# Optimization experiments

Measured on AMD Instinct MI355X. Metric: run time of the kernel, lower is better.

Reference implementation:

```python
import jax, jax.numpy as jnp
import numpy as np

B, SQ, SK, D, H = 4, 2048, 2048, 1024, 16
EPS = 1e-6  # flax LayerNorm default


def layer_norm(x, g, b):
    m = x.mean(-1, keepdims=True)
    var = ((x - m) ** 2).mean(-1, keepdims=True)
    return (x - m) * jax.lax.rsqrt(var + EPS) * g + b


def setup_inputs() -> dict:
    key = jax.random.key(0)
    ks = jax.random.split(key, 16)
    s = 1.0 / np.sqrt(D).astype(np.float32)
    inp = {
        'q': jax.random.normal(ks[0], (B, SQ, D), jnp.float32),
        'k': jax.random.normal(ks[1], (B, SK, D), jnp.float32),
        'v': jax.random.normal(ks[2], (B, SK, D), jnp.float32),
        'mask': jax.random.randint(ks[3], (B, SK), 0, 2).astype(bool),
        'Wq': jax.random.normal(ks[4], (D, D), jnp.float32) * s,
        'bq': jnp.zeros((D,), jnp.float32),
        'Wk': jax.random.normal(ks[5], (D, D), jnp.float32) * s,
        'bk': jnp.zeros((D,), jnp.float32),
        'Wv': jax.random.normal(ks[6], (D, D), jnp.float32) * s,
        'bv': jnp.zeros((D,), jnp.float32),
        'Wo': jax.random.normal(ks[7], (D, D), jnp.float32) * s,
        'bo': jnp.zeros((D,), jnp.float32),
        'g1': jnp.ones((D,), jnp.float32),
        'b1': jnp.zeros((D,), jnp.float32),
        'g2': jnp.ones((D,), jnp.float32),
        'b2': jnp.zeros((D,), jnp.float32),
    }
    return inp


def reference(q, k, v, mask, Wq, bq, Wk, bk, Wv, bv, Wo, bo, g1, b1, g2, b2):
    qp = q @ Wq + bq                      # [B, SQ, D]
    kp = k @ Wk + bk                      # [B, SK, D]
    vp = v @ Wv + bv
    qh = qp.reshape(B, SQ, H, D // H)     # head = slice of last dim (matches scatter)
    kh = kp.reshape(B, SK, H, D // H)
    vh = vp.reshape(B, SK, H, D // H)
    # NOTE: original scales by sqrt(dim_out) (full dim), not head dim
    logits = jnp.einsum('bqhd,bkhd->bhqk', qh, kh) / np.sqrt(D).astype(np.float32)
    m = mask[:, None, None, :]            # [B,1,1,SK] broadcast over heads & queries
    A = jax.nn.softmax(jnp.where(m, logits, -jnp.inf), axis=-1)
    A = jnp.where(jnp.isnan(A), 0.0, A)   # fully-masked rows -> 0 (as in original)
    attn = jnp.einsum('bhqk,bkhd->bqhd', A, vh).reshape(B, SQ, D)  # gather heads
    x = layer_norm(qp + attn, g1, b1)
    out = layer_norm(x + jax.nn.relu(x @ Wo + bo), g2, b2)
    return out
```

## Files before the change

kernel.cpp:

```cpp
#include <hip/hip_runtime.h>

#define B_   4
#define SQS  2048
#define SKS  2048
#define DM   1024
#define H_   16
#define MT   8192

typedef __attribute__((ext_vector_type(8))) short bf16x8;
typedef __attribute__((ext_vector_type(4))) float f32x4;

__device__ __forceinline__ float bf2f(unsigned int u) { return __uint_as_float(u << 16); }
__device__ __forceinline__ unsigned short f2bf(float f) {
  unsigned int u = __float_as_uint(f);
  return (unsigned short)((u + 0x7fffu + ((u >> 16) & 1u)) >> 16);
}
__device__ __forceinline__ unsigned int pk_bf16(float a, float b) {
  return __builtin_amdgcn_perm(__float_as_uint(b) + 0x8000u,
                               __float_as_uint(a) + 0x8000u, 0x07060302u);
}
__device__ __forceinline__ void async16(const void* g, void* l) {
  __builtin_amdgcn_global_load_lds((const __attribute__((address_space(1))) unsigned int*)g,
                                   (__attribute__((address_space(3))) unsigned int*)l,
                                   16, 0, 0);
}

__global__ __launch_bounds__(256)
void cvt3_kernel(const float* __restrict__ a, const float* __restrict__ b,
                 const float* __restrict__ c,
                 unsigned short* __restrict__ oa, unsigned short* __restrict__ ob,
                 unsigned short* __restrict__ oc)
{
  const float* src = (blockIdx.y == 0) ? a : (blockIdx.y == 1) ? b : c;
  unsigned short* dst = (blockIdx.y == 0) ? oa : (blockIdx.y == 1) ? ob : oc;
  size_t i = ((size_t)blockIdx.x * 256 + threadIdx.x) * 4;
  float4 f = *(const float4*)(src + i);
  uint2 o;
  o.x = (unsigned)f2bf(f.x) | ((unsigned)f2bf(f.y) << 16);
  o.y = (unsigned)f2bf(f.z) | ((unsigned)f2bf(f.w) << 16);
  *(uint2*)(dst + i) = o;
}

__global__ __launch_bounds__(256)
void wtrans_kernel(const float* __restrict__ w0, const float* __restrict__ w1,
                   const float* __restrict__ w2, const float* __restrict__ w3,
                   unsigned short* __restrict__ t0, unsigned short* __restrict__ t1,
                   unsigned short* __restrict__ t2, unsigned short* __restrict__ t3)
{
  const float* W = (blockIdx.z == 0) ? w0 : (blockIdx.z == 1) ? w1 : (blockIdx.z == 2) ? w2 : w3;
  unsigned short* Wt = (blockIdx.z == 0) ? t0 : (blockIdx.z == 1) ? t1 : (blockIdx.z == 2) ? t2 : t3;
  __shared__ float s[32][33];
  int n0 = blockIdx.x * 32, k0 = blockIdx.y * 32;
  int tid = threadIdx.x;
#pragma unroll
  for (int p = 0; p < 4; p++) {
    int idx = p * 256 + tid;
    int r = idx >> 5, c = idx & 31;
    s[r][c] = W[(size_t)(k0 + r) * DM + n0 + c];
  }
  __syncthreads();
#pragma unroll
  for (int p = 0; p < 4; p++) {
    int idx = p * 256 + tid;
    int r = idx >> 5, c = idx & 31;
    Wt[(size_t)(n0 + r) * DM + k0 + c] = f2bf(s[c][r]);
  }
}

__global__ __launch_bounds__(256)
void mkbias_kernel(const int* __restrict__ m, float* __restrict__ bias)
{
  int i = blockIdx.x * 256 + threadIdx.x;
  bias[i] = m[i] ? 0.0f : -1e30f;
}

__global__ __launch_bounds__(256)
void qkv_gemm(const unsigned short* __restrict__ A0, const unsigned short* __restrict__ A1,
              const unsigned short* __restrict__ A2,
              const unsigned short* __restrict__ W0, const unsigned short* __restrict__ W1,
              const unsigned short* __restrict__ W2,
              const float* __restrict__ s0, const float* __restrict__ s1,
              const float* __restrict__ s2,
              unsigned short* __restrict__ o0, unsigned short* __restrict__ o1,
              unsigned short* __restrict__ o2)
{
  const int z = blockIdx.z;
  const unsigned short* A  = (z == 0) ? A0 : (z == 1) ? A1 : A2;
  const unsigned short* Wt = (z == 0) ? W0 : (z == 1) ? W1 : W2;
  const float* bias        = (z == 0) ? s0 : (z == 1) ? s1 : s2;
  unsigned short* C        = (z == 0) ? o0 : (z == 1) ? o1 : o2;

  __shared__ short As[128 * 32];
  __shared__ short Bs[128 * 32];
  const int tid = threadIdx.x;
  const int m0 = blockIdx.y * 128, n0 = blockIdx.x * 128;
  const int wave = tid >> 6, ln = tid & 15, qd = (tid & 63) >> 4;
  const int wm = (wave >> 1) * 64, wn = (wave & 1) * 64;
  const int cA = tid, cB = 256 + tid;
  const int arA = cA >> 2, acA = (cA & 3) * 8;
  const int arB = cB >> 2, acB = (cB & 3) * 8;

  f32x4 acc[4][4];
  const f32x4 vzero = {0.f, 0.f, 0.f, 0.f};
#pragma unroll
  for (int i = 0; i < 4; i++)
#pragma unroll
    for (int j = 0; j < 4; j++) acc[i][j] = vzero;

  for (int k0 = 0; k0 < DM; k0 += 32) {
    __syncthreads();
    async16(A  + (size_t)(m0 + arA) * DM + k0 + acA, (char*)As + cA * 16);
    async16(A  + (size_t)(m0 + arB) * DM + k0 + acB, (char*)As + cB * 16);
    async16(Wt + (size_t)(n0 + arA) * DM + k0 + acA, (char*)Bs + cA * 16);
    async16(Wt + (size_t)(n0 + arB) * DM + k0 + acB, (char*)Bs + cB * 16);
    __syncthreads();

    bf16x8 af[4], bfr[4];
#pragma unroll
    for (int i = 0; i < 4; i++)
      af[i] = *(const bf16x8*)(As + (wm + i * 16 + ln) * 32 + qd * 8);
#pragma unroll
    for (int j = 0; j < 4; j++)
      bfr[j] = *(const bf16x8*)(Bs + (wn + j * 16 + ln) * 32 + qd * 8);
#pragma unroll
    for (int i = 0; i < 4; i++)
#pragma unroll
      for (int j = 0; j < 4; j++)
        acc[i][j] = __builtin_amdgcn_mfma_f32_16x16x32_bf16(af[i], bfr[j], acc[i][j], 0, 0, 0);
  }

#pragma unroll
  for (int j = 0; j < 4; j++) {
    int col = n0 + wn + j * 16 + ln;
    float bj = bias[col];
#pragma unroll
    for (int i = 0; i < 4; i++) {
      int row = m0 + wm + i * 16 + qd * 4;
#pragma unroll
      for (int r = 0; r < 4; r++)
        C[(size_t)(row + r) * DM + col] = f2bf(acc[i][j][r] + bj);
    }
  }
}

__global__ __launch_bounds__(256)
void gemm_bf16(const unsigned short* __restrict__ A,
               const unsigned short* __restrict__ Wt,
               const float* __restrict__ bias,
               unsigned short* __restrict__ C,
               int relu)
{
  __shared__ short As[128 * 32];
  __shared__ short Bs[128 * 32];
  const int tid = threadIdx.x;
  const int m0 = blockIdx.y * 128, n0 = blockIdx.x * 128;
  const int wave = tid >> 6, ln = tid & 15, qd = (tid & 63) >> 4;
  const int wm = (wave >> 1) * 64, wn = (wave & 1) * 64;
  const int cA = tid, cB = 256 + tid;
  const int arA = cA >> 2, acA = (cA & 3) * 8;
  const int arB = cB >> 2, acB = (cB & 3) * 8;

  f32x4 acc[4][4];
  const f32x4 vzero = {0.f, 0.f, 0.f, 0.f};
#pragma unroll
  for (int i = 0; i < 4; i++)
#pragma unroll
    for (int j = 0; j < 4; j++) acc[i][j] = vzero;

  for (int k0 = 0; k0 < DM; k0 += 32) {
    __syncthreads();
    async16(A  + (size_t)(m0 + arA) * DM + k0 + acA, (char*)As + cA * 16);
    async16(A  + (size_t)(m0 + arB) * DM + k0 + acB, (char*)As + cB * 16);
    async16(Wt + (size_t)(n0 + arA) * DM + k0 + acA, (char*)Bs + cA * 16);
    async16(Wt + (size_t)(n0 + arB) * DM + k0 + acB, (char*)Bs + cB * 16);
    __syncthreads();

    bf16x8 af[4], bfr[4];
#pragma unroll
    for (int i = 0; i < 4; i++)
      af[i] = *(const bf16x8*)(As + (wm + i * 16 + ln) * 32 + qd * 8);
#pragma unroll
    for (int j = 0; j < 4; j++)
      bfr[j] = *(const bf16x8*)(Bs + (wn + j * 16 + ln) * 32 + qd * 8);
#pragma unroll
    for (int i = 0; i < 4; i++)
#pragma unroll
      for (int j = 0; j < 4; j++)
        acc[i][j] = __builtin_amdgcn_mfma_f32_16x16x32_bf16(af[i], bfr[j], acc[i][j], 0, 0, 0);
  }

#pragma unroll
  for (int j = 0; j < 4; j++) {
    int col = n0 + wn + j * 16 + ln;
    float bj = bias[col];
#pragma unroll
    for (int i = 0; i < 4; i++) {
      int row = m0 + wm + i * 16 + qd * 4;
#pragma unroll
      for (int r = 0; r < 4; r++) {
        float v = acc[i][j][r] + bj;
        if (relu) v = fmaxf(v, 0.f);
        C[(size_t)(row + r) * DM + col] = f2bf(v);
      }
    }
  }
}

__global__ __launch_bounds__(256)
void vtrans_kernel(const unsigned short* __restrict__ vp, unsigned short* __restrict__ vT)
{
  __shared__ unsigned short s[64][68];
  int b = blockIdx.z, h = blockIdx.y, k0 = blockIdx.x * 64;
  int tid = threadIdx.x;
#pragma unroll
  for (int p = 0; p < 4; p++) {
    int c = p * 256 + tid;
    int k = c >> 4, d0 = (c & 15) * 4;
    uint2 u = *(const uint2*)(vp + (size_t)(b * SKS + k0 + k) * DM + (h << 6) + d0);
    *(uint2*)(&s[k][d0]) = u;
  }
  __syncthreads();
#pragma unroll
  for (int p = 0; p < 4; p++) {
    int c = p * 256 + tid;
    int d = c >> 4, m = c & 15;
    int t  = ((m & 1) << 1) | (m >> 3);
    int qd = (m >> 1) & 3;
    int ks = t * 16 + qd * 4;
    unsigned short r0 = s[ks + 0][d];
    unsigned short r1 = s[ks + 1][d];
    unsigned short r2 = s[ks + 2][d];
    unsigned short r3 = s[ks + 3][d];
    uint2 u;
    u.x = (unsigned)r0 | ((unsigned)r1 << 16);
    u.y = (unsigned)r2 | ((unsigned)r3 << 16);
    *(uint2*)(vT + (size_t)((b * H_ + h) * 64 + d) * SKS + k0 + m * 4) = u;
  }
}

__global__ __launch_bounds__(256, 4)
void attn_fwd(const unsigned short* __restrict__ qp,
              const unsigned short* __restrict__ kp,
              const unsigned short* __restrict__ vT,
              const float* __restrict__ maskb,
              unsigned short* __restrict__ attn)
{
  __shared__ short Ks[64 * 64];
  __shared__ short Vs[64 * 64];
  __shared__ float bias_s[64];

  const int tid = threadIdx.x;
  const int b = blockIdx.z, h = blockIdx.y, q0 = blockIdx.x * 128;
  const int wave = tid >> 6, ln = tid & 15, qd = (tid & 63) >> 4;
  const int cA = tid, cB = 256 + tid;
  const int rA = cA >> 3, jgA = ((cA & 7) ^ (rA & 7)) * 8;
  const int rB = cB >> 3, jgB = ((cB & 7) ^ (rB & 7)) * 8;
  const float SCALE = 0.03125f;

  const unsigned short* kbase = kp + (size_t)(b * SKS) * DM + (h << 6);
  const unsigned short* vbase = vT + (size_t)((b * H_ + h) * 64) * SKS;

  const unsigned short* qrow = qp + (size_t)(b * SQS + q0 + wave * 32 + ln) * DM + (h << 6);
  bf16x8 qf[2][2];
  qf[0][0] = *(const bf16x8*)(qrow + qd * 8);
  qf[0][1] = *(const bf16x8*)(qrow + 32 + qd * 8);
  qf[1][0] = *(const bf16x8*)(qrow + 16 * DM + qd * 8);
  qf[1][1] = *(const bf16x8*)(qrow + 16 * DM + 32 + qd * 8);

  const f32x4 vzero = {0.f, 0.f, 0.f, 0.f};
  f32x4 oA[2][4];
#pragma unroll
  for (int g = 0; g < 2; g++)
#pragma unroll
    for (int t = 0; t < 4; t++) oA[g][t] = vzero;
  float lr[2] = {0.f, 0.f};

  for (int kt = 0; kt < SKS / 64; kt++) {
    const int k0 = kt * 64;
    __syncthreads();
    if (tid < 64) bias_s[tid] = maskb[b * SKS + k0 + tid];
    async16(kbase + (size_t)(k0 + rA) * DM + jgA, (char*)Ks + cA * 16);
    async16(kbase + (size_t)(k0 + rB) * DM + jgB, (char*)Ks + cB * 16);
    async16(vbase + (size_t)rA * SKS + k0 + jgA, (char*)Vs + cA * 16);
    async16(vbase + (size_t)rB * SKS + k0 + jgB, (char*)Vs + cB * 16);
    __syncthreads();

    f32x4 sS[2][4];
#pragma unroll
    for (int t = 0; t < 4; t++) {
      const short* krow = Ks + (t * 16 + ln) * 64;
      bf16x8 kf0 = *(const bf16x8*)(krow + ((0 + qd) ^ (ln & 7)) * 8);
      bf16x8 kf1 = *(const bf16x8*)(krow + ((4 + qd) ^ (ln & 7)) * 8);
      f32x4 a0 = __builtin_amdgcn_mfma_f32_16x16x32_bf16(kf0, qf[0][0], vzero, 0, 0, 0);
      a0       = __builtin_amdgcn_mfma_f32_16x16x32_bf16(kf1, qf[0][1], a0,    0, 0, 0);
      f32x4 a1 = __builtin_amdgcn_mfma_f32_16x16x32_bf16(kf0, qf[1][0], vzero, 0, 0, 0);
      a1       = __builtin_amdgcn_mfma_f32_16x16x32_bf16(kf1, qf[1][1], a1,    0, 0, 0);
      sS[0][t] = a0;
      sS[1][t] = a1;
    }

    bf16x8 pf[2][2];
#pragma unroll
    for (int g = 0; g < 2; g++) {
      float p[4][4];
      float acc = 0.f;
#pragma unroll
      for (int t = 0; t < 4; t++) {
        float4 bt = *(const float4*)(bias_s + t * 16 + qd * 4);
        p[t][0] = __expf(fmaf(sS[g][t][0], SCALE, bt.x));
        p[t][1] = __expf(fmaf(sS[g][t][1], SCALE, bt.y));
        p[t][2] = __expf(fmaf(sS[g][t][2], SCALE, bt.z));
        p[t][3] = __expf(fmaf(sS[g][t][3], SCALE, bt.w));
        acc += (p[t][0] + p[t][1]) + (p[t][2] + p[t][3]);
      }
      lr[g] += acc;
      union { bf16x8 v; unsigned int u[4]; } P0, P1;
      P0.u[0] = pk_bf16(p[0][0], p[0][1]);
      P0.u[1] = pk_bf16(p[0][2], p[0][3]);
      P0.u[2] = pk_bf16(p[2][0], p[2][1]);
      P0.u[3] = pk_bf16(p[2][2], p[2][3]);
      P1.u[0] = pk_bf16(p[1][0], p[1][1]);
      P1.u[1] = pk_bf16(p[1][2], p[1][3]);
      P1.u[2] = pk_bf16(p[3][0], p[3][1]);
      P1.u[3] = pk_bf16(p[3][2], p[3][3]);
      pf[g][0] = P0.v;
      pf[g][1] = P1.v;
    }

#pragma unroll
    for (int t2 = 0; t2 < 4; t2++) {
      const short* vrow = Vs + (t2 * 16 + ln) * 64;
#pragma unroll
      for (int kk = 0; kk < 2; kk++) {
        bf16x8 vf = *(const bf16x8*)(vrow + ((kk * 4 + qd) ^ (ln & 7)) * 8);
        oA[0][t2] = __builtin_amdgcn_mfma_f32_16x16x32_bf16(pf[0][kk], vf, oA[0][t2], 0, 0, 0);
        oA[1][t2] = __builtin_amdgcn_mfma_f32_16x16x32_bf16(pf[1][kk], vf, oA[1][t2], 0, 0, 0);
      }
    }
  }

#pragma unroll
  for (int g = 0; g < 2; g++) {
    float l = lr[g];
    l += __shfl_xor(l, 16);
    l += __shfl_xor(l, 32);
    float linv[4];
#pragma unroll
    for (int r = 0; r < 4; r++) {
      float lq = __shfl(l, qd * 4 + r);
      linv[r] = (lq > 0.f) ? 1.0f / lq : 0.f;
    }
#pragma unroll
    for (int t2 = 0; t2 < 4; t2++)
#pragma unroll
      for (int r = 0; r < 4; r++) {
        size_t idx = (size_t)(b * SQS + q0 + wave * 32 + g * 16 + qd * 4 + r) * DM
                   + (h << 6) + t2 * 16 + ln;
        attn[idx] = f2bf(oA[g][t2][r] * linv[r]);
      }
  }
}

__global__ __launch_bounds__(256)
void ln_fuse(const unsigned short* __restrict__ Xa, const unsigned short* __restrict__ Xb,
             const float* __restrict__ gamma, const float* __restrict__ beta,
             unsigned short* __restrict__ outb, float* __restrict__ outf, int mode)
{
  const int row = blockIdx.x, tid = threadIdx.x;
  const size_t base = (size_t)row * DM + tid * 4;
  uint2 ua = *(const uint2*)(Xa + base);
  uint2 ub = *(const uint2*)(Xb + base);
  float v0 = bf2f(ua.x & 0xffffu) + bf2f(ub.x & 0xffffu);
  float v1 = bf2f(ua.x >> 16)     + bf2f(ub.x >> 16);
  float v2 = bf2f(ua.y & 0xffffu) + bf2f(ub.y & 0xffffu);
  float v3 = bf2f(ua.y >> 16)     + bf2f(ub.y >> 16);
  float s  = (v0 + v1) + (v2 + v3);
  float s2 = (v0 * v0 + v1 * v1) + (v2 * v2 + v3 * v3);
#pragma unroll
  for (int off = 1; off < 64; off <<= 1) {
    s  += __shfl_xor(s, off);
    s2 += __shfl_xor(s2, off);
  }
  __shared__ float red[8];
  if ((tid & 63) == 0) { red[tid >> 6] = s; red[4 + (tid >> 6)] = s2; }
  __syncthreads();
  float S  = (red[0] + red[1]) + (red[2] + red[3]);
  float S2 = (red[4] + red[5]) + (red[6] + red[7]);
  float mean = S * (1.0f / 1024.0f);
  float var  = S2 * (1.0f / 1024.0f) - mean * mean;
  float rstd = rsqrtf(var + 1e-6f);
  int c = tid * 4;
  float o0 = (v0 - mean) * rstd * gamma[c + 0] + beta[c + 0];
  float o1 = (v1 - mean) * rstd * gamma[c + 1] + beta[c + 1];
  float o2 = (v2 - mean) * rstd * gamma[c + 2] + beta[c + 2];
  float o3 = (v3 - mean) * rstd * gamma[c + 3] + beta[c + 3];
  if (mode == 0) {
    uint2 o;
    o.x = (unsigned)f2bf(o0) | ((unsigned)f2bf(o1) << 16);
    o.y = (unsigned)f2bf(o2) | ((unsigned)f2bf(o3) << 16);
    *(uint2*)(outb + base) = o;
  } else {
    float4 o = {o0, o1, o2, o3};
    *(float4*)(outf + base) = o;
  }
}

extern "C" void kernel_launch(void* const* d_in, const int* in_sizes, int n_in,
                              void* d_out, int out_size, void* d_ws, size_t ws_size,
                              hipStream_t stream)
{
  (void)in_sizes; (void)n_in; (void)out_size; (void)ws_size;
  const float* q    = (const float*)d_in[0];
  const float* k    = (const float*)d_in[1];
  const float* v    = (const float*)d_in[2];
  const int*   mask = (const int*)  d_in[3];
  const float* Wq   = (const float*)d_in[4];
  const float* bq   = (const float*)d_in[5];
  const float* Wk   = (const float*)d_in[6];
  const float* bk   = (const float*)d_in[7];
  const float* Wv   = (const float*)d_in[8];
  const float* bv   = (const float*)d_in[9];
  const float* Wo   = (const float*)d_in[10];
  const float* bo   = (const float*)d_in[11];
  const float* g1   = (const float*)d_in[12];
  const float* b1   = (const float*)d_in[13];
  const float* g2   = (const float*)d_in[14];
  const float* b2   = (const float*)d_in[15];

  char* ws = (char*)d_ws;
  const size_t SZ16 = (size_t)16 << 20;
  unsigned short* qi   = (unsigned short*)(ws + 0 * SZ16);
  unsigned short* ki   = (unsigned short*)(ws + 1 * SZ16);
  unsigned short* vi   = (unsigned short*)(ws + 2 * SZ16);
  unsigned short* qpb  = (unsigned short*)(ws + 3 * SZ16);
  unsigned short* kpb  = (unsigned short*)(ws + 4 * SZ16);
  unsigned short* vpb  = (unsigned short*)(ws + 5 * SZ16);
  unsigned short* vTb  = (unsigned short*)(ws + 6 * SZ16);
  unsigned short* Wqt  = (unsigned short*)(ws + 7 * SZ16 + ((size_t)0 << 20));
  unsigned short* Wkt  = (unsigned short*)(ws + 7 * SZ16 + ((size_t)2 << 20));
  unsigned short* Wvt  = (unsigned short*)(ws + 7 * SZ16 + ((size_t)4 << 20));
  unsigned short* Wot  = (unsigned short*)(ws + 7 * SZ16 + ((size_t)6 << 20));
  float*          mskb = (float*)         (ws + 7 * SZ16 + ((size_t)8 << 20));
  unsigned short* attnb = qi;
  unsigned short* xb    = ki;
  unsigned short* hb    = vi;

  cvt3_kernel  <<<dim3(8192, 3),    256, 0, stream>>>(q, k, v, qi, ki, vi);
  wtrans_kernel<<<dim3(32, 32, 4),  256, 0, stream>>>(Wq, Wk, Wv, Wo, Wqt, Wkt, Wvt, Wot);
  mkbias_kernel<<<32,               256, 0, stream>>>(mask, mskb);

  qkv_gemm     <<<dim3(8, 64, 3),   256, 0, stream>>>(qi, ki, vi, Wqt, Wkt, Wvt,
                                                      bq, bk, bv, qpb, kpb, vpb);

  vtrans_kernel<<<dim3(32, 16, 4),  256, 0, stream>>>(vpb, vTb);
  attn_fwd     <<<dim3(16, 16, 4),  256, 0, stream>>>(qpb, kpb, vTb, mskb, attnb);

  ln_fuse      <<<8192,             256, 0, stream>>>(qpb, attnb, g1, b1, xb, nullptr, 0);
  gemm_bf16    <<<dim3(8, 64),      256, 0, stream>>>(xb, Wot, bo, hb, 1);
  ln_fuse      <<<8192,             256, 0, stream>>>(xb, hb, g2, b2, nullptr, (float*)d_out, 1);
}
```

Before: 391.1 us.

## Widen GEMM and attention K-tiles, fold scale into K projection, use exp2

Doubles the K-step of both GEMMs to 64 with an XOR-swizzled LDS layout, and doubles the attention key tile to 128 per iteration. This halves the number of barrier round trips. The softmax scale and log2(e) are folded into the K projection output and the mask bias. The bias is injected as the MFMA accumulator init, so the kernel can use native exp2 and truncating bf16 packing. Row sums are now computed with an MFMA against a ones vector instead of shuffle reductions. Truncating P to bf16 and computing the row sum from bf16 values change numerics slightly. The bigger tiles raise LDS use per block.

New measurement: 374.4 us. 1.04x faster.

```diff
diff --git a/kernel.cpp b/kernel.cpp
--- a/kernel.cpp
+++ b/kernel.cpp
@@ -15,15 +15,24 @@
   unsigned int u = __float_as_uint(f);
   return (unsigned short)((u + 0x7fffu + ((u >> 16) & 1u)) >> 16);
 }
-__device__ __forceinline__ unsigned int pk_bf16(float a, float b) {
-  return __builtin_amdgcn_perm(__float_as_uint(b) + 0x8000u,
-                               __float_as_uint(a) + 0x8000u, 0x07060302u);
+__device__ __forceinline__ unsigned int pk_trunc(float a, float b) {
+  return __builtin_amdgcn_perm(__float_as_uint(b), __float_as_uint(a), 0x07060302u);
+}
+__device__ __forceinline__ float fexp2(float x) {
+#if __has_builtin(__builtin_amdgcn_exp2f)
+  return __builtin_amdgcn_exp2f(x);
+#else
+  return __expf(x * 0.69314718056f);
+#endif
 }
 __device__ __forceinline__ void async16(const void* g, void* l) {
   __builtin_amdgcn_global_load_lds((const __attribute__((address_space(1))) unsigned int*)g,
                                    (__attribute__((address_space(3))) unsigned int*)l,
                                    16, 0, 0);
 }
+
+#define KSCALE 0.0450842200f
+#define BIAS_UNMASKED 0.0028151213f
 
 __global__ __launch_bounds__(256)
 void cvt3_kernel(const float* __restrict__ a, const float* __restrict__ b,
@@ -71,7 +80,7 @@
 void mkbias_kernel(const int* __restrict__ m, float* __restrict__ bias)
 {
   int i = blockIdx.x * 256 + threadIdx.x;
-  bias[i] = m[i] ? 0.0f : -1e30f;
+  bias[i] = m[i] ? BIAS_UNMASKED : -1e30f;
 }
 
 __global__ __launch_bounds__(256)
@@ -89,16 +98,22 @@
   const unsigned short* Wt = (z == 0) ? W0 : (z == 1) ? W1 : W2;
   const float* bias        = (z == 0) ? s0 : (z == 1) ? s1 : s2;
   unsigned short* C        = (z == 0) ? o0 : (z == 1) ? o1 : o2;
-
-  __shared__ short As[128 * 32];
-  __shared__ short Bs[128 * 32];
+  const float sc           = (z == 1) ? KSCALE : 1.0f;
+
+  __shared__ short As[128 * 64];
+  __shared__ short Bs[128 * 64];
   const int tid = threadIdx.x;
   const int m0 = blockIdx.y * 128, n0 = blockIdx.x * 128;
   const int wave = tid >> 6, ln = tid & 15, qd = (tid & 63) >> 4;
   const int wm = (wave >> 1) * 64, wn = (wave & 1) * 64;
-  const int cA = tid, cB = 256 + tid;
-  const int arA = cA >> 2, acA = (cA & 3) * 8;
-  const int arB = cB >> 2, acB = (cB & 3) * 8;
+
+  int srow[4], sgj[4];
+#pragma unroll
+  for (int u = 0; u < 4; u++) {
+    int c = u * 256 + tid;
+    srow[u] = c >> 3;
+    sgj[u] = ((c & 7) ^ (srow[u] & 7)) * 8;
+  }
 
   f32x4 acc[4][4];
   const f32x4 vzero = {0.f, 0.f, 0.f, 0.f};
@@ -107,26 +122,32 @@
 #pragma unroll
     for (int j = 0; j < 4; j++) acc[i][j] = vzero;
 
-  for (int k0 = 0; k0 < DM; k0 += 32) {
+  for (int k0 = 0; k0 < DM; k0 += 64) {
     __syncthreads();
-    async16(A  + (size_t)(m0 + arA) * DM + k0 + acA, (char*)As + cA * 16);
-    async16(A  + (size_t)(m0 + arB) * DM + k0 + acB, (char*)As + cB * 16);
-    async16(Wt + (size_t)(n0 + arA) * DM + k0 + acA, (char*)Bs + cA * 16);
-    async16(Wt + (size_t)(n0 + arB) * DM + k0 + acB, (char*)Bs + cB * 16);
+#pragma unroll
+    for (int u = 0; u < 4; u++) {
+      int c = u * 256 + tid;
+      async16(A  + (size_t)(m0 + srow[u]) * DM + k0 + sgj[u], (char*)As + c * 16);
+      async16(Wt + (size_t)(n0 + srow[u]) * DM + k0 + sgj[u], (char*)Bs + c * 16);
+    }
     __syncthreads();
 
-    bf16x8 af[4], bfr[4];
-#pragma unroll
-    for (int i = 0; i < 4; i++)
-      af[i] = *(const bf16x8*)(As + (wm + i * 16 + ln) * 32 + qd * 8);
-#pragma unroll
-    for (int j = 0; j < 4; j++)
-      bfr[j] = *(const bf16x8*)(Bs + (wn + j * 16 + ln) * 32 + qd * 8);
-#pragma unroll
-    for (int i = 0; i < 4; i++)
+#pragma unroll
+    for (int kk = 0; kk < 2; kk++) {
+      const int ch = ((kk * 4 + qd) ^ (ln & 7)) * 8;
+      bf16x8 af[4], bfr[4];
+#pragma unroll
+      for (int i = 0; i < 4; i++)
+        af[i] = *(const bf16x8*)(As + (wm + i * 16 + ln) * 64 + ch);
 #pragma unroll
       for (int j = 0; j < 4; j++)
-        acc[i][j] = __builtin_amdgcn_mfma_f32_16x16x32_bf16(af[i], bfr[j], acc[i][j], 0, 0, 0);
+        bfr[j] = *(const bf16x8*)(Bs + (wn + j * 16 + ln) * 64 + ch);
+#pragma unroll
+      for (int i = 0; i < 4; i++)
+#pragma unroll
+        for (int j = 0; j < 4; j++)
+          acc[i][j] = __builtin_amdgcn_mfma_f32_16x16x32_bf16(af[i], bfr[j], acc[i][j], 0, 0, 0);
+    }
   }
 
 #pragma unroll
@@ -138,7 +159,7 @@
       int row = m0 + wm + i * 16 + qd * 4;
 #pragma unroll
       for (int r = 0; r < 4; r++)
-        C[(size_t)(row + r) * DM + col] = f2bf(acc[i][j][r] + bj);
+        C[(size_t)(row + r) * DM + col] = f2bf((acc[i][j][r] + bj) * sc);
     }
   }
 }
@@ -150,15 +171,20 @@
                unsigned short* __restrict__ C,
                int relu)
 {
-  __shared__ short As[128 * 32];
-  __shared__ short Bs[128 * 32];
+  __shared__ short As[128 * 64];
+  __shared__ short Bs[128 * 64];
   const int tid = threadIdx.x;
   const int m0 = blockIdx.y * 128, n0 = blockIdx.x * 128;
   const int wave = tid >> 6, ln = tid & 15, qd = (tid & 63) >> 4;
   const int wm = (wave >> 1) * 64, wn = (wave & 1) * 64;
-  const int cA = tid, cB = 256 + tid;
-  const int arA = cA >> 2, acA = (cA & 3) * 8;
-  const int arB = cB >> 2, acB = (cB & 3) * 8;
+
+  int srow[4], sgj[4];
+#pragma unroll
+  for (int u = 0; u < 4; u++) {
+    int c = u * 256 + tid;
+    srow[u] = c >> 3;
+    sgj[u] = ((c & 7) ^ (srow[u] & 7)) * 8;
+  }
 
   f32x4 acc[4][4];
   const f32x4 vzero = {0.f, 0.f, 0.f, 0.f};
@@ -167,26 +193,32 @@
 #pragma unroll
     for (int j = 0; j < 4; j++) acc[i][j] = vzero;
 
-  for (int k0 = 0; k0 < DM; k0 += 32) {
+  for (int k0 = 0; k0 < DM; k0 += 64) {
     __syncthreads();
-    async16(A  + (size_t)(m0 + arA) * DM + k0 + acA, (char*)As + cA * 16);
-    async16(A  + (size_t)(m0 + arB) * DM + k0 + acB, (char*)As + cB * 16);
-    async16(Wt + (size_t)(n0 + arA) * DM + k0 + acA, (char*)Bs + cA * 16);
-    async16(Wt + (size_t)(n0 + arB) * DM + k0 + acB, (char*)Bs + cB * 16);
+#pragma unroll
+    for (int u = 0; u < 4; u++) {
+      int c = u * 256 + tid;
+      async16(A  + (size_t)(m0 + srow[u]) * DM + k0 + sgj[u], (char*)As + c * 16);
+      async16(Wt + (size_t)(n0 + srow[u]) * DM + k0 + sgj[u], (char*)Bs + c * 16);
+    }
     __syncthreads();
 
-    bf16x8 af[4], bfr[4];
-#pragma unroll
-    for (int i = 0; i < 4; i++)
-      af[i] = *(const bf16x8*)(As + (wm + i * 16 + ln) * 32 + qd * 8);
-#pragma unroll
-    for (int j = 0; j < 4; j++)
-      bfr[j] = *(const bf16x8*)(Bs + (wn + j * 16 + ln) * 32 + qd * 8);
-#pragma unroll
-    for (int i = 0; i < 4; i++)
+#pragma unroll
+    for (int kk = 0; kk < 2; kk++) {
+      const int ch = ((kk * 4 + qd) ^ (ln & 7)) * 8;
+      bf16x8 af[4], bfr[4];
+#pragma unroll
+      for (int i = 0; i < 4; i++)
+        af[i] = *(const bf16x8*)(As + (wm + i * 16 + ln) * 64 + ch);
 #pragma unroll
       for (int j = 0; j < 4; j++)
-        acc[i][j] = __builtin_amdgcn_mfma_f32_16x16x32_bf16(af[i], bfr[j], acc[i][j], 0, 0, 0);
+        bfr[j] = *(const bf16x8*)(Bs + (wn + j * 16 + ln) * 64 + ch);
+#pragma unroll
+      for (int i = 0; i < 4; i++)
+#pragma unroll
+        for (int j = 0; j < 4; j++)
+          acc[i][j] = __builtin_amdgcn_mfma_f32_16x16x32_bf16(af[i], bfr[j], acc[i][j], 0, 0, 0);
+    }
   }
 
 #pragma unroll
@@ -245,17 +277,24 @@
               const float* __restrict__ maskb,
               unsigned short* __restrict__ attn)
 {
-  __shared__ short Ks[64 * 64];
-  __shared__ short Vs[64 * 64];
-  __shared__ float bias_s[64];
+  __shared__ short Ks[128 * 64];
+  __shared__ short Vs[64 * 128];
+  __shared__ float bias_s[128];
 
   const int tid = threadIdx.x;
   const int b = blockIdx.z, h = blockIdx.y, q0 = blockIdx.x * 128;
   const int wave = tid >> 6, ln = tid & 15, qd = (tid & 63) >> 4;
-  const int cA = tid, cB = 256 + tid;
-  const int rA = cA >> 3, jgA = ((cA & 7) ^ (rA & 7)) * 8;
-  const int rB = cB >> 3, jgB = ((cB & 7) ^ (rB & 7)) * 8;
-  const float SCALE = 0.03125f;
+
+  int kRow[4], kOff[4], vRow[4], vOff[4];
+#pragma unroll
+  for (int u = 0; u < 4; u++) {
+    int c = u * 256 + tid;
+    kRow[u] = c >> 3;
+    kOff[u] = ((c & 7) ^ (kRow[u] & 7)) * 8;
+    vRow[u] = c >> 4;
+    int j = c & 15;
+    vOff[u] = ((j & 8) | ((j ^ vRow[u]) & 7)) * 8;
+  }
 
   const unsigned short* kbase = kp + (size_t)(b * SKS) * DM + (h << 6);
   const unsigned short* vbase = vT + (size_t)((b * H_ + h) * 64) * SKS;
@@ -267,89 +306,92 @@
   qf[1][0] = *(const bf16x8*)(qrow + 16 * DM + qd * 8);
   qf[1][1] = *(const bf16x8*)(qrow + 16 * DM + 32 + qd * 8);
 
+  union { bf16x8 v; unsigned int u[4]; } onesf;
+  onesf.u[0] = onesf.u[1] = onesf.u[2] = onesf.u[3] = 0x3F803F80u;
+
   const f32x4 vzero = {0.f, 0.f, 0.f, 0.f};
-  f32x4 oA[2][4];
-#pragma unroll
-  for (int g = 0; g < 2; g++)
+  f32x4 oA[2][4], lacc[2];
+#pragma unroll
+  for (int g = 0; g < 2; g++) {
+    lacc[g] = vzero;
 #pragma unroll
     for (int t = 0; t < 4; t++) oA[g][t] = vzero;
-  float lr[2] = {0.f, 0.f};
-
-  for (int kt = 0; kt < SKS / 64; kt++) {
-    const int k0 = kt * 64;
+  }
+
+  for (int kt = 0; kt < SKS / 128; kt++) {
+    const int k0 = kt * 128;
     __syncthreads();
-    if (tid < 64) bias_s[tid] = maskb[b * SKS + k0 + tid];
-    async16(kbase + (size_t)(k0 + rA) * DM + jgA, (char*)Ks + cA * 16);
-    async16(kbase + (size_t)(k0 + rB) * DM + jgB, (char*)Ks + cB * 16);
-    async16(vbase + (size_t)rA * SKS + k0 + jgA, (char*)Vs + cA * 16);
-    async16(vbase + (size_t)rB * SKS + k0 + jgB, (char*)Vs + cB * 16);
+    if (tid < 128) bias_s[tid] = maskb[b * SKS + k0 + tid];
+#pragma unroll
+    for (int u = 0; u < 4; u++) {
+      int c = u * 256 + tid;
+      async16(kbase + (size_t)(k0 + kRow[u]) * DM + kOff[u], (char*)Ks + c * 16);
+      async16(vbase + (size_t)vRow[u] * SKS + k0 + vOff[u], (char*)Vs + c * 16);
+    }
     __syncthreads();
 
-    f32x4 sS[2][4];
-#pragma unroll
-    for (int t = 0; t < 4; t++) {
-      const short* krow = Ks + (t * 16 + ln) * 64;
-      bf16x8 kf0 = *(const bf16x8*)(krow + ((0 + qd) ^ (ln & 7)) * 8);
-      bf16x8 kf1 = *(const bf16x8*)(krow + ((4 + qd) ^ (ln & 7)) * 8);
-      f32x4 a0 = __builtin_amdgcn_mfma_f32_16x16x32_bf16(kf0, qf[0][0], vzero, 0, 0, 0);
-      a0       = __builtin_amdgcn_mfma_f32_16x16x32_bf16(kf1, qf[0][1], a0,    0, 0, 0);
-      f32x4 a1 = __builtin_amdgcn_mfma_f32_16x16x32_bf16(kf0, qf[1][0], vzero, 0, 0, 0);
-      a1       = __builtin_amdgcn_mfma_f32_16x16x32_bf16(kf1, qf[1][1], a1,    0, 0, 0);
-      sS[0][t] = a0;
-      sS[1][t] = a1;
-    }
-
-    bf16x8 pf[2][2];
-#pragma unroll
-    for (int g = 0; g < 2; g++) {
-      float p[4][4];
-      float acc = 0.f;
+#pragma unroll
+    for (int h2 = 0; h2 < 2; h2++) {
+      f32x4 sS[2][4];
 #pragma unroll
       for (int t = 0; t < 4; t++) {
-        float4 bt = *(const float4*)(bias_s + t * 16 + qd * 4);
-        p[t][0] = __expf(fmaf(sS[g][t][0], SCALE, bt.x));
-        p[t][1] = __expf(fmaf(sS[g][t][1], SCALE, bt.y));
-        p[t][2] = __expf(fmaf(sS[g][t][2], SCALE, bt.z));
-        p[t][3] = __expf(fmaf(sS[g][t][3], SCALE, bt.w));
-        acc += (p[t][0] + p[t][1]) + (p[t][2] + p[t][3]);
+        const short* krow = Ks + (h2 * 64 + t * 16 + ln) * 64;
+        bf16x8 kf0 = *(const bf16x8*)(krow + ((0 + qd) ^ (ln & 7)) * 8);
+        bf16x8 kf1 = *(const bf16x8*)(krow + ((4 + qd) ^ (ln & 7)) * 8);
+        f32x4 btv = *(const f32x4*)(bias_s + h2 * 64 + t * 16 + qd * 4);
+        f32x4 a0 = __builtin_amdgcn_mfma_f32_16x16x32_bf16(kf0, qf[0][0], btv, 0, 0, 0);
+        a0       = __builtin_amdgcn_mfma_f32_16x16x32_bf16(kf1, qf[0][1], a0,  0, 0, 0);
+        f32x4 a1 = __builtin_amdgcn_mfma_f32_16x16x32_bf16(kf0, qf[1][0], btv, 0, 0, 0);
+        a1       = __builtin_amdgcn_mfma_f32_16x16x32_bf16(kf1, qf[1][1], a1,  0, 0, 0);
+        sS[0][t] = a0;
+        sS[1][t] = a1;
       }
-      lr[g] += acc;
-      union { bf16x8 v; unsigned int u[4]; } P0, P1;
-      P0.u[0] = pk_bf16(p[0][0], p[0][1]);
-      P0.u[1] = pk_bf16(p[0][2], p[0][3]);
-      P0.u[2] = pk_bf16(p[2][0], p[2][1]);
-      P0.u[3] = pk_bf16(p[2][2], p[2][3]);
-      P1.u[0] = pk_bf16(p[1][0], p[1][1]);
-      P1.u[1] = pk_bf16(p[1][2], p[1][3]);
-      P1.u[2] = pk_bf16(p[3][0], p[3][1]);
-      P1.u[3] = pk_bf16(p[3][2], p[3][3]);
-      pf[g][0] = P0.v;
-      pf[g][1] = P1.v;
-    }
-
-#pragma unroll
-    for (int t2 = 0; t2 < 4; t2++) {
-      const short* vrow = Vs + (t2 * 16 + ln) * 64;
-#pragma unroll
-      for (int kk = 0; kk < 2; kk++) {
-        bf16x8 vf = *(const bf16x8*)(vrow + ((kk * 4 + qd) ^ (ln & 7)) * 8);
-        oA[0][t2] = __builtin_amdgcn_mfma_f32_16x16x32_bf16(pf[0][kk], vf, oA[0][t2], 0, 0, 0);
-        oA[1][t2] = __builtin_amdgcn_mfma_f32_16x16x32_bf16(pf[1][kk], vf, oA[1][t2], 0, 0, 0);
+
+      bf16x8 pf[2][2];
+#pragma unroll
+      for (int g = 0; g < 2; g++) {
+        float p[4][4];
+#pragma unroll
+        for (int t = 0; t < 4; t++) {
+          p[t][0] = fexp2(sS[g][t][0]);
+          p[t][1] = fexp2(sS[g][t][1]);
+          p[t][2] = fexp2(sS[g][t][2]);
+          p[t][3] = fexp2(sS[g][t][3]);
+        }
+        union { bf16x8 v; unsigned int u[4]; } P0, P1;
+        P0.u[0] = pk_trunc(p[0][0], p[0][1]);
+        P0.u[1] = pk_trunc(p[0][2], p[0][3]);
+        P0.u[2] = pk_trunc(p[2][0], p[2][1]);
+        P0.u[3] = pk_trunc(p[2][2], p[2][3]);
+        P1.u[0] = pk_trunc(p[1][0], p[1][1]);
+        P1.u[1] = pk_trunc(p[1][2], p[1][3]);
+        P1.u[2] = pk_trunc(p[3][0], p[3][1]);
+        P1.u[3] = pk_trunc(p[3][2], p[3][3]);
+        pf[g][0] = P0.v;
+        pf[g][1] = P1.v;
+        lacc[g] = __builtin_amdgcn_mfma_f32_16x16x32_bf16(pf[g][0], onesf.v, lacc[g], 0, 0, 0);
+        lacc[g] = __builtin_amdgcn_mfma_f32_16x16x32_bf16(pf[g][1], onesf.v, lacc[g], 0, 0, 0);
       }
+
+#pragma unroll
+      for (int t2 = 0; t2 < 4; t2++) {
+        const short* vrow = Vs + (t2 * 16 + ln) * 128;
+#pragma unroll
+        for (int kk = 0; kk < 2; kk++) {
+          bf16x8 vf = *(const bf16x8*)(vrow + (h2 * 8 + ((kk * 4 + qd) ^ (ln & 7))) * 8);
+          oA[0][t2] = __builtin_amdgcn_mfma_f32_16x16x32_bf16(pf[0][kk], vf, oA[0][t2], 0, 0, 0);
+          oA[1][t2] = __builtin_amdgcn_mfma_f32_16x16x32_bf16(pf[1][kk], vf, oA[1][t2], 0, 0, 0);
+        }
+      }
     }
   }
 
 #pragma unroll
   for (int g = 0; g < 2; g++) {
-    float l = lr[g];
-    l += __shfl_xor(l, 16);
-    l += __shfl_xor(l, 32);
     float linv[4];
 #pragma unroll
-    for (int r = 0; r < 4; r++) {
-      float lq = __shfl(l, qd * 4 + r);
-      linv[r] = (lq > 0.f) ? 1.0f / lq : 0.f;
-    }
+    for (int r = 0; r < 4; r++)
+      linv[r] = (lacc[g][r] > 0.f) ? 1.0f / lacc[g][r] : 0.f;
 #pragma unroll
     for (int t2 = 0; t2 < 4; t2++)
 #pragma unroll
```
